# Kernel optimization log

Measured on AMD Instinct MI355X. Metric: run time of the kernel, lower is better.

## Reference

```python
import jax, jax.numpy as jnp
import numpy as np

INFO = 32  # info_dim


def _resort_perm(new_shape, cluster, old_num_cols):
    # Replicates resort(): column c of resort_mat has its single 1 at row perm[c],
    # so x @ resort_mat == x[..., perm]. (Faithfully reproduces the original
    # old_idx arithmetic, including its old_num_cols choice.)
    n0, n1 = new_shape
    perm = np.zeros(n0 * n1, np.int32)
    counter = 0
    for i in range(n0):
        for j in range(n1):
            filter_idx = (i % cluster[0]) * cluster[0] + (j % cluster[1])
            cluster_idx = (i // cluster[0]) * (n1 // cluster[1]) + (j // cluster[1])
            perm[counter] = filter_idx * old_num_cols + cluster_idx
            counter += 1
    return perm


def setup_inputs() -> dict:
    key = jax.random.key(0)
    ks = iter(jax.random.split(key, 64))
    def w(shape, scale=0.1):
        return jax.random.normal(next(ks), shape, dtype=jnp.float32) * scale
    B = 512
    inp = {"channel": jax.random.normal(next(ks), (B, 10, 16), dtype=jnp.float32)}
    for name, cin in [("l1", 10), ("g1", 10), ("l2", 2 * INFO), ("g2", 2 * INFO),
                      ("l4", 2 * INFO), ("g4", 2 * INFO), ("l5", 2 * INFO), ("g5", 2 * INFO),
                      ("l7", 2 * INFO), ("g7", 2 * INFO)]:
        inp["w_" + name] = w((INFO, cin))
        inp["b_" + name] = w((INFO,))
    for name in ["l3", "g3", "l6", "g6"]:
        inp["w_" + name] = w((9, INFO, 2 * INFO))
        inp["b_" + name] = w((9, INFO))
    inp["w_l8"] = w((1, 2 * INFO))
    inp["b_l8"] = w((1,))
    inp["perm3"] = jnp.asarray(_resort_perm((12, 12), (3, 3), 12))
    inp["perm6"] = jnp.asarray(_resort_perm((36, 36), (3, 3), 108))
    return inp


def _conv1(x, w, b):  # 1x1 Conv1d: [B,C,N] x [O,C] -> [B,O,N]
    return jnp.einsum('bcn,oc->bon', x, w) + b[None, :, None]


def _mean_bcast(x):
    # x @ (ones(N,N)/N) == broadcast mean over width (global_info_... = True)
    return jnp.broadcast_to(x.mean(axis=-1, keepdims=True), x.shape)


def _process_layer(x, wl, bl, wg, bg):
    fl = jax.nn.relu(_conv1(x, wl, bl))
    fg = _mean_bcast(jax.nn.relu(_conv1(x, wg, bg)))
    return jnp.concatenate([fl, fg], axis=1)


def _process_interp(x, wl, bl, wg, bg, perm):
    # wl/wg: [9,O,C]; per-filter [B,2*INFO,N] outputs concatenated along width,
    # then resorted (the one-hot permutation matmul becomes a gather).
    fl = jax.nn.relu(jnp.einsum('bcn,foc->fbon', x, wl) + bl[:, None, :, None])
    fg = _mean_bcast(jax.nn.relu(jnp.einsum('bcn,foc->fbon', x, wg) + bg[:, None, :, None]))
    cat = jnp.concatenate([fl, fg], axis=2)  # [9,B,2*INFO,N]
    f, b, c, n = cat.shape
    wide = jnp.transpose(cat, (1, 2, 0, 3)).reshape(b, c, f * n)  # [B,2*INFO,9N]
    return wide[:, :, perm]


def reference(channel, w_l1, b_l1, w_g1, b_g1, w_l2, b_l2, w_g2, b_g2,
              w_l3, b_l3, w_g3, b_g3, w_l4, b_l4, w_g4, b_g4,
              w_l5, b_l5, w_g5, b_g5, w_l6, b_l6, w_g6, b_g6,
              w_l7, b_l7, w_g7, b_g7, w_l8, b_l8, perm3, perm6):
    f = _process_layer(channel, w_l1, b_l1, w_g1, b_g1)        # [B,64,16]
    f = _process_layer(f, w_l2, b_l2, w_g2, b_g2)              # [B,64,16]
    f = _process_interp(f, w_l3, b_l3, w_g3, b_g3, perm3)      # [B,64,144]
    f = _process_layer(f, w_l4, b_l4, w_g4, b_g4)              # [B,64,144]
    f = _process_layer(f, w_l5, b_l5, w_g5, b_g5)              # [B,64,144]
    f = _process_interp(f, w_l6, b_l6, w_g6, b_g6, perm6)      # [B,64,1296]
    f = _process_layer(f, w_l7, b_l7, w_g7, b_g7)              # [B,64,1296]
    return _conv1(f, w_l8, b_l8) * np.pi                       # [B,1,1296]
```

## Files before the change

### kernel.cpp

```cpp
#include <hip/hip_runtime.h>
#include <math.h>

#define PI_F 3.14159265358979323846f
#define XQS 580
#define XB_B 4640

__device__ __forceinline__ void conv32K(
    const float* __restrict__ Wh,
    const float* __restrict__ xin,
    float* __restrict__ xout,
    const float* __restrict__ m0, const float* __restrict__ m1, const float* __restrict__ m2,
    const float* __restrict__ m3, const float* __restrict__ m4, const float* __restrict__ m5,
    float* __restrict__ xmsOut, int lane, int wid_u)
{
    int isg = wid_u >= 4, rb = (wid_u & 3) * 8;
    int rowbase = isg * 32 + rb;
    int cA = lane, cB = 64 + lane, cC = 128 + (lane & 15);
    float a0[8], a1[8], a2[8], a3[8], a4[8], a5[8];
    #pragma unroll
    for (int i = 0; i < 8; ++i) { a0[i]=0.f;a1[i]=0.f;a2[i]=0.f;a3[i]=0.f;a4[i]=0.f;a5[i]=0.f; }
    #pragma unroll 1
    for (int kb = 0; kb < 4; ++kb) {
        int ca = kb*2, cb = kb*2 + 1;
        float4 xA0 = *(const float4*)&xin[ca*XQS + cA*4];
        float4 xA1 = *(const float4*)&xin[cb*XQS + cA*4];
        float4 xB0 = *(const float4*)&xin[ca*XQS + cB*4];
        float4 xB1 = *(const float4*)&xin[cb*XQS + cB*4];
        float4 xC0 = *(const float4*)&xin[ca*XQS + cC*4];
        float4 xC1 = *(const float4*)&xin[cb*XQS + cC*4];
        float4 yA0 = *(const float4*)&xin[XB_B + ca*XQS + cA*4];
        float4 yA1 = *(const float4*)&xin[XB_B + cb*XQS + cA*4];
        float4 yB0 = *(const float4*)&xin[XB_B + ca*XQS + cB*4];
        float4 yB1 = *(const float4*)&xin[XB_B + cb*XQS + cB*4];
        float4 yC0 = *(const float4*)&xin[XB_B + ca*XQS + cC*4];
        float4 yC1 = *(const float4*)&xin[XB_B + cb*XQS + cC*4];
        const float* wb = Wh + rowbase*32 + kb*8;
        #pragma unroll
        for (int oi = 0; oi < 8; ++oi) {
            float4 w0 = *(const float4*)&wb[oi*32];
            float4 w1 = *(const float4*)&wb[oi*32 + 4];
            a0[oi] = fmaf(w0.x,xA0.x,a0[oi]); a0[oi] = fmaf(w0.y,xA0.y,a0[oi]);
            a0[oi] = fmaf(w0.z,xA0.z,a0[oi]); a0[oi] = fmaf(w0.w,xA0.w,a0[oi]);
            a0[oi] = fmaf(w1.x,xA1.x,a0[oi]); a0[oi] = fmaf(w1.y,xA1.y,a0[oi]);
            a0[oi] = fmaf(w1.z,xA1.z,a0[oi]); a0[oi] = fmaf(w1.w,xA1.w,a0[oi]);
            a1[oi] = fmaf(w0.x,xB0.x,a1[oi]); a1[oi] = fmaf(w0.y,xB0.y,a1[oi]);
            a1[oi] = fmaf(w0.z,xB0.z,a1[oi]); a1[oi] = fmaf(w0.w,xB0.w,a1[oi]);
            a1[oi] = fmaf(w1.x,xB1.x,a1[oi]); a1[oi] = fmaf(w1.y,xB1.y,a1[oi]);
            a1[oi] = fmaf(w1.z,xB1.z,a1[oi]); a1[oi] = fmaf(w1.w,xB1.w,a1[oi]);
            a2[oi] = fmaf(w0.x,xC0.x,a2[oi]); a2[oi] = fmaf(w0.y,xC0.y,a2[oi]);
            a2[oi] = fmaf(w0.z,xC0.z,a2[oi]); a2[oi] = fmaf(w0.w,xC0.w,a2[oi]);
            a2[oi] = fmaf(w1.x,xC1.x,a2[oi]); a2[oi] = fmaf(w1.y,xC1.y,a2[oi]);
            a2[oi] = fmaf(w1.z,xC1.z,a2[oi]); a2[oi] = fmaf(w1.w,xC1.w,a2[oi]);
            a3[oi] = fmaf(w0.x,yA0.x,a3[oi]); a3[oi] = fmaf(w0.y,yA0.y,a3[oi]);
            a3[oi] = fmaf(w0.z,yA0.z,a3[oi]); a3[oi] = fmaf(w0.w,yA0.w,a3[oi]);
            a3[oi] = fmaf(w1.x,yA1.x,a3[oi]); a3[oi] = fmaf(w1.y,yA1.y,a3[oi]);
            a3[oi] = fmaf(w1.z,yA1.z,a3[oi]); a3[oi] = fmaf(w1.w,yA1.w,a3[oi]);
            a4[oi] = fmaf(w0.x,yB0.x,a4[oi]); a4[oi] = fmaf(w0.y,yB0.y,a4[oi]);
            a4[oi] = fmaf(w0.z,yB0.z,a4[oi]); a4[oi] = fmaf(w0.w,yB0.w,a4[oi]);
            a4[oi] = fmaf(w1.x,yB1.x,a4[oi]); a4[oi] = fmaf(w1.y,yB1.y,a4[oi]);
            a4[oi] = fmaf(w1.z,yB1.z,a4[oi]); a4[oi] = fmaf(w1.w,yB1.w,a4[oi]);
            a5[oi] = fmaf(w0.x,yC0.x,a5[oi]); a5[oi] = fmaf(w0.y,yC0.y,a5[oi]);
            a5[oi] = fmaf(w0.z,yC0.z,a5[oi]); a5[oi] = fmaf(w0.w,yC0.w,a5[oi]);
            a5[oi] = fmaf(w1.x,yC1.x,a5[oi]); a5[oi] = fmaf(w1.y,yC1.y,a5[oi]);
            a5[oi] = fmaf(w1.z,yC1.z,a5[oi]); a5[oi] = fmaf(w1.w,yC1.w,a5[oi]);
        }
    }
    #pragma unroll
    for (int oi = 0; oi < 8; ++oi) {
        int row = rowbase + oi;
        a0[oi] = fmaxf(a0[oi] + m0[row], 0.f);
        a1[oi] = fmaxf(a1[oi] + m1[row], 0.f);
        a2[oi] = fmaxf(a2[oi] + m2[row], 0.f);
        a3[oi] = fmaxf(a3[oi] + m3[row], 0.f);
        a4[oi] = fmaxf(a4[oi] + m4[row], 0.f);
        a5[oi] = fmaxf(a5[oi] + m5[row], 0.f);
    }
    if (!isg) {
        int q0 = rb >> 2;
        *(float4*)&xout[ q0   *XQS + cA*4] = make_float4(a0[0],a0[1],a0[2],a0[3]);
        *(float4*)&xout[(q0+1)*XQS + cA*4] = make_float4(a0[4],a0[5],a0[6],a0[7]);
        *(float4*)&xout[ q0   *XQS + cB*4] = make_float4(a1[0],a1[1],a1[2],a1[3]);
        *(float4*)&xout[(q0+1)*XQS + cB*4] = make_float4(a1[4],a1[5],a1[6],a1[7]);
        *(float4*)&xout[XB_B +  q0   *XQS + cA*4] = make_float4(a3[0],a3[1],a3[2],a3[3]);
        *(float4*)&xout[XB_B + (q0+1)*XQS + cA*4] = make_float4(a3[4],a3[5],a3[6],a3[7]);
        *(float4*)&xout[XB_B +  q0   *XQS + cB*4] = make_float4(a4[0],a4[1],a4[2],a4[3]);
        *(float4*)&xout[XB_B + (q0+1)*XQS + cB*4] = make_float4(a4[4],a4[5],a4[6],a4[7]);
        if (lane < 16) {
            *(float4*)&xout[ q0   *XQS + cC*4] = make_float4(a2[0],a2[1],a2[2],a2[3]);
            *(float4*)&xout[(q0+1)*XQS + cC*4] = make_float4(a2[4],a2[5],a2[6],a2[7]);
            *(float4*)&xout[XB_B +  q0   *XQS + cC*4] = make_float4(a5[0],a5[1],a5[2],a5[3]);
            *(float4*)&xout[XB_B + (q0+1)*XQS + cC*4] = make_float4(a5[4],a5[5],a5[6],a5[7]);
        }
    } else {
        #pragma unroll
        for (int oi = 0; oi < 8; ++oi) {
            float s0 = a0[oi] + a1[oi] + ((lane < 16) ? a2[oi] : 0.f);
            float s1 = a3[oi] + a4[oi] + ((lane < 16) ? a5[oi] : 0.f);
            #pragma unroll
            for (int off = 1; off < 64; off <<= 1) { s0 += __shfl_xor(s0, off); s1 += __shfl_xor(s1, off); }
            if (lane == 0) { xmsOut[rb + oi] = s0 * (1.f/144.f); xmsOut[32 + rb + oi] = s1 * (1.f/144.f); }
        }
    }
}

__global__ __launch_bounds__(512, 2) void kfull(
    const float* __restrict__ ch,
    const float* __restrict__ wl1, const float* __restrict__ bl1,
    const float* __restrict__ wg1, const float* __restrict__ bg1,
    const float* __restrict__ wl2, const float* __restrict__ bl2,
    const float* __restrict__ wg2, const float* __restrict__ bg2,
    const float* __restrict__ wl3, const float* __restrict__ bl3,
    const float* __restrict__ wg3, const float* __restrict__ bg3,
    const float* __restrict__ wl4, const float* __restrict__ bl4,
    const float* __restrict__ wg4, const float* __restrict__ bg4,
    const float* __restrict__ wl5, const float* __restrict__ bl5,
    const float* __restrict__ wg5, const float* __restrict__ bg5,
    const float* __restrict__ wl6, const float* __restrict__ bl6,
    const float* __restrict__ wg6, const float* __restrict__ bg6,
    const float* __restrict__ wl7, const float* __restrict__ bl7,
    const float* __restrict__ wg7, const float* __restrict__ bg7,
    const float* __restrict__ wl8, const float* __restrict__ bl8,
    const int* __restrict__ perm3, const int* __restrict__ perm6,
    float* __restrict__ out)
{
    __shared__ float U[14336];
    __shared__ float xB[9280];
    __shared__ float W45h[4096];
    __shared__ float W7s[2048];
    __shared__ float mp4[896];
    __shared__ float mp5[128];
    __shared__ float mp6[448];
    __shared__ float mpg6[448];
    __shared__ float sgf[896];
    __shared__ float g6m[448];
    __shared__ float wl8s[64];
    __shared__ float xms4[64];
    __shared__ float xms5[64];
    __shared__ float l8v[2016];
    __shared__ int   pml[1296];
    __shared__ int   cnt[1008];
    __shared__ int   pfn3[144];
    __shared__ float redbuf[16];
    __shared__ float CbS[2];

    const int tid = threadIdx.x, lane = tid & 63, wid = tid >> 6;
    const int blk = blockIdx.x;
    const int wid_u = __builtin_amdgcn_readfirstlane(wid);

    float* f1s   = U;
    float* gts   = U + 2048;
    float* f2l   = U + 3072;
    float* cat3T = U + 5120;
    float* g3m   = U + 12352;
    float* xls   = U + 12814;
    float* x4s   = U;
    float* wg6h  = U;
    float* wl6h  = U + 7168;

    for (int t = tid; t < 1024; t += 512) {
        int l = t >> 9, rem = t & 511;
        int row = rem >> 3, q = rem & 7;
        const float* src = l ? ((row < 32) ? wl5 + row*64 : wg5 + (row-32)*64)
                             : ((row < 32) ? wl4 + row*64 : wg4 + (row-32)*64);
        *(float4*)&W45h[l*2048 + row*32 + q*4] = *(const float4*)&src[q*4];
    }
    {
        int row = tid >> 3, q = tid & 7;
        const float* src = (row < 32) ? (wl7 + row*64) : (wg7 + (row-32)*64);
        *(float4*)&W7s[row*32 + q*4] = *(const float4*)&src[q*4];
    }
    if (tid < 64) wl8s[tid] = wl8[tid];
    if (tid < 320) { int b = tid >= 160, i = tid - b*160; xls[b*160 + i] = ch[(2*blk + b)*160 + i]; }
    if (tid < 144) pfn3[tid] = perm3[tid];
    for (int t = tid; t < 1008; t += 512) cnt[t] = 0;
    __syncthreads();

    for (int t = tid; t < 1296; t += 512) { int p = perm6[t]; pml[t] = p; atomicAdd(&cnt[p], 1); }
    #pragma unroll
    for (int it = 0; it < 4; ++it) {
        int t = tid + it*512; int b = t >> 10, o = (t >> 4) & 63, n = t & 15;
        int isg = o >= 32, oo = o & 31;
        const float* w = isg ? wg1 : wl1;
        float acc = (isg ? bg1 : bl1)[oo];
        #pragma unroll
        for (int c = 0; c < 10; ++c) acc = fmaf(w[oo*10+c], xls[b*160 + c*16+n], acc);
        acc = fmaxf(acc, 0.f);
        if (isg) gts[b*512 + oo*16+n] = acc; else f1s[b*1024 + o*16+n] = acc;
    }
    __syncthreads();
    if (tid < 64) {
        int b = tid >> 5, j = tid & 31;
        float s = 0.f;
        #pragma unroll
        for (int n = 0; n < 16; ++n) s += gts[b*512 + j*16+n];
        s *= (1.f/16.f);
        #pragma unroll
        for (int n = 0; n < 16; ++n) f1s[b*1024 + (32+j)*16+n] = s;
    }
    __syncthreads();

    #pragma unroll
    for (int it = 0; it < 4; ++it) {
        int t = tid + it*512; int b = t >> 10, o = (t >> 4) & 63, n = t & 15;
        int isg = o >= 32, oo = o & 31;
        const float* w = isg ? wg2 : wl2;
        float acc = (isg ? bg2 : bl2)[oo];
        #pragma unroll
        for (int c = 0; c < 64; ++c) acc = fmaf(w[oo*64+c], f1s[b*1024 + c*16+n], acc);
        acc = fmaxf(acc, 0.f);
        if (isg) gts[b*512 + oo*16+n] = acc; else f2l[b*1024 + o*16+n] = acc;
    }
    __syncthreads();
    if (tid < 64) {
        int b = tid >> 5, j = tid & 31;
        float s = 0.f;
        #pragma unroll
        for (int n = 0; n < 16; ++n) s += gts[b*512 + j*16+n];
        s *= (1.f/16.f);
        #pragma unroll
        for (int n = 0; n < 16; ++n) f2l[b*1024 + (32+j)*16+n] = s;
    }
    __syncthreads();

    {
        int n16 = lane & 15, cs = lane >> 4;
        float xr0[16], xr1[16];
        #pragma unroll
        for (int i = 0; i < 16; ++i) {
            xr0[i] = f2l[cs*256 + i*16 + n16];
            xr1[i] = f2l[1024 + cs*256 + i*16 + n16];
        }
        int isg = wid_u >= 4;
        #pragma unroll 2
        for (int k = 0; k < 56; ++k) {
            int r = wid_u*56 + k;
            int rr = isg ? r - 224 : r;
            const float* wrow = (isg ? wg3 : wl3) + rr*64 + cs*16;
            float p0 = 0.f, p1 = 0.f;
            #pragma unroll
            for (int q = 0; q < 4; ++q) {
                float4 w = ((const float4*)wrow)[q];
                p0 = fmaf(w.x, xr0[q*4+0], p0); p0 = fmaf(w.y, xr0[q*4+1], p0);
                p0 = fmaf(w.z, xr0[q*4+2], p0); p0 = fmaf(w.w, xr0[q*4+3], p0);
                p1 = fmaf(w.x, xr1[q*4+0], p1); p1 = fmaf(w.y, xr1[q*4+1], p1);
                p1 = fmaf(w.z, xr1[q*4+2], p1); p1 = fmaf(w.w, xr1[q*4+3], p1);
            }
            p0 += __shfl_xor(p0, 16); p0 += __shfl_xor(p0, 32);
            p1 += __shfl_xor(p1, 16); p1 += __shfl_xor(p1, 32);
            float bb = (isg ? bg3 : bl3)[rr];
            p0 = fmaxf(p0 + bb, 0.f); p1 = fmaxf(p1 + bb, 0.f);
            if (!isg) {
                if (cs == 0) { cat3T[n16*226 + rr] = p0; cat3T[3616 + n16*226 + rr] = p1; }
            } else {
                p0 += __shfl_xor(p0, 1); p0 += __shfl_xor(p0, 2);
                p0 += __shfl_xor(p0, 4); p0 += __shfl_xor(p0, 8);
                p1 += __shfl_xor(p1, 1); p1 += __shfl_xor(p1, 2);
                p1 += __shfl_xor(p1, 4); p1 += __shfl_xor(p1, 8);
                if (lane == 0) {
                    g3m[(rr >> 5)*33 + (rr & 31)] = p0 * (1.f/16.f);
                    g3m[231 + (rr >> 5)*33 + (rr & 31)] = p1 * (1.f/16.f);
                }
            }
        }
    }
    __syncthreads();

    for (int t = tid; t < 9216; t += 512) {
        int b = t / 4608, rem = t - b*4608;
        int c4 = rem / 576, r2 = rem - c4*576;
        int col = r2 >> 2, ci = r2 & 3, c = c4*4 + ci;
        int p3 = pfn3[col]; int pf = p3 >> 4, pn = p3 & 15;
        xB[b*XB_B + c4*XQS + col*4 + ci] = cat3T[b*3616 + pn*226 + pf*32 + c];
    }
    for (int t = tid; t < 896; t += 512) {
        int b = t >= 448, t2 = t - b*448;
        int pf = t2 >> 6, row = t2 & 63;
        const float* w = ((row < 32) ? wl4 + row*64 : wg4 + (row-32)*64) + 32;
        float s = (row < 32) ? bl4[row] : bg4[row-32];
        #pragma unroll
        for (int q = 0; q < 8; ++q) {
            float4 wv = ((const float4*)w)[q];
            s = fmaf(wv.x, g3m[b*231 + pf*33 + q*4+0], s);
            s = fmaf(wv.y, g3m[b*231 + pf*33 + q*4+1], s);
            s = fmaf(wv.z, g3m[b*231 + pf*33 + q*4+2], s);
            s = fmaf(wv.w, g3m[b*231 + pf*33 + q*4+3], s);
        }
        mp4[b*448 + pf*64 + row] = s;
    }
    __syncthreads();

    {
        int pA = pfn3[lane] >> 4;
        int pB = pfn3[64 + lane] >> 4;
        int pC = pfn3[128 + (lane & 15)] >> 4;
        conv32K(W45h, xB, x4s,
                mp4 + pA*64, mp4 + pB*64, mp4 + pC*64,
                mp4 + 448 + pA*64, mp4 + 448 + pB*64, mp4 + 448 + pC*64,
                xms4, lane, wid_u);
    }
    __syncthreads();
    if (tid < 128) {
        int b = tid >= 64, row = tid & 63;
        const float* w = ((row < 32) ? wl5 + row*64 : wg5 + (row-32)*64) + 32;
        float s = (row < 32) ? bl5[row] : bg5[row-32];
        #pragma unroll
        for (int q = 0; q < 8; ++q) {
            float4 wv = ((const float4*)w)[q];
            s = fmaf(wv.x, xms4[b*32 + q*4+0], s);
            s = fmaf(wv.y, xms4[b*32 + q*4+1], s);
            s = fmaf(wv.z, xms4[b*32 + q*4+2], s);
            s = fmaf(wv.w, xms4[b*32 + q*4+3], s);
        }
        mp5[tid] = s;
    }
    __syncthreads();
    conv32K(W45h + 2048, x4s, xB,
            mp5, mp5, mp5, mp5 + 64, mp5 + 64, mp5 + 64,
            xms5, lane, wid_u);
    __syncthreads();

    #pragma unroll
    for (int k = 0; k < 7; ++k) {
        int t = tid + k*512;
        int half = t >= 1792, t2 = t - half*1792;
        int row = t2 >> 3, q = t2 & 7;
        const float* src = half ? (wl6 + row*64) : (wg6 + row*64);
        *(float4*)&U[half*7168 + row*32 + q*4] = *(const float4*)&src[q*4];
    }
    for (int t = tid; t < 896; t += 512) {
        int b = t >= 448, t2 = t - b*448;
        int isw = t2 >= 224, row = t2 - isw*224;
        const float* w = (isw ? wl6 + row*64 : wg6 + row*64) + 32;
        float s = isw ? bl6[row] : bg6[row];
        #pragma unroll
        for (int q = 0; q < 8; ++q) {
            float4 wv = ((const float4*)w)[q];
            s = fmaf(wv.x, xms5[b*32 + q*4+0], s);
            s = fmaf(wv.y, xms5[b*32 + q*4+1], s);
            s = fmaf(wv.z, xms5[b*32 + q*4+2], s);
            s = fmaf(wv.w, xms5[b*32 + q*4+3], s);
        }
        if (isw) mp6[b*224 + row] = s; else mpg6[b*224 + row] = s;
    }
    __syncthreads();

    {
        int bb = wid_u >= 4, w4 = wid_u & 3;
        int r0 = w4 * 56;
        int c0 = lane, c1 = 64 + lane, c2 = 128 + (lane & 15);
        const float* xb = xB + bb*XB_B;
        float4 xc0[8], xc1[8], xc2[8];
        #pragma unroll
        for (int q = 0; q < 8; ++q) {
            xc0[q] = *(const float4*)&xb[q*XQS + c0*4];
            xc1[q] = *(const float4*)&xb[q*XQS + c1*4];
            xc2[q] = *(const float4*)&xb[q*XQS + c2*4];
        }
        #pragma unroll 1
        for (int k = 0; k < 56; ++k) {
            int r = r0 + k;
            const float* wr = wg6h + r*32;
            float bb0 = mpg6[bb*224 + r];
            float v0 = bb0, v1 = bb0, v2 = bb0;
            #pragma unroll
            for (int q = 0; q < 8; ++q) {
                float4 w = *(const float4*)&wr[q*4];
                v0 = fmaf(w.x,xc0[q].x,v0); v0 = fmaf(w.y,xc0[q].y,v0); v0 = fmaf(w.z,xc0[q].z,v0); v0 = fmaf(w.w,xc0[q].w,v0);
                v1 = fmaf(w.x,xc1[q].x,v1); v1 = fmaf(w.y,xc1[q].y,v1); v1 = fmaf(w.z,xc1[q].z,v1); v1 = fmaf(w.w,xc1[q].w,v1);
                v2 = fmaf(w.x,xc2[q].x,v2); v2 = fmaf(w.y,xc2[q].y,v2); v2 = fmaf(w.z,xc2[q].z,v2); v2 = fmaf(w.w,xc2[q].w,v2);
            }
            float s = fmaxf(v0,0.f) + fmaxf(v1,0.f) + ((lane < 16) ? fmaxf(v2,0.f) : 0.f);
            #pragma unroll
            for (int off = 1; off < 64; off <<= 1) s += __shfl_xor(s, off);
            if (lane == 0) g6m[bb*224 + r] = s * (1.f/144.f);
        }
    }
    __syncthreads();

    for (int t = tid; t < 896; t += 512) {
        int b = t >= 448, t2 = t - b*448;
        int f = t2 >> 6, o7 = t2 & 63;
        const float* w = ((o7 < 32) ? wl7 + o7*64 : wg7 + (o7-32)*64) + 32;
        float s = (o7 < 32) ? bl7[o7] : bg7[o7-32];
        #pragma unroll
        for (int q = 0; q < 8; ++q) {
            float4 wv = ((const float4*)w)[q];
            s = fmaf(wv.x, g6m[b*224 + f*32 + q*4+0], s);
            s = fmaf(wv.y, g6m[b*224 + f*32 + q*4+1], s);
            s = fmaf(wv.z, g6m[b*224 + f*32 + q*4+2], s);
            s = fmaf(wv.w, g6m[b*224 + f*32 + q*4+3], s);
        }
        sgf[b*448 + f*64 + o7] = s;
    }
    __syncthreads();

    float gacc0 = 0.f, gacc1 = 0.f;
    {
        int t = 8*wid_u + (lane >> 3);
        bool valid = t < 63;
        int tt = valid ? t : 62;
        int f = tt / 9, g = tt - f*9;
        int colA = g*16 + (lane & 7), colB = colA + 8;
        const float* wfh = wl6h + f*1024;

        float a0A[32], a0B[32], a1A[32], a1B[32];
        #pragma unroll
        for (int o = 0; o < 32; ++o) { a0A[o]=0.f; a0B[o]=0.f; a1A[o]=0.f; a1B[o]=0.f; }
        #pragma unroll 1
        for (int kb = 0; kb < 4; ++kb) {
            int ca = kb*2, cb = kb*2 + 1;
            float4 xA0 = *(const float4*)&xB[ca*XQS + colA*4];
            float4 xA1 = *(const float4*)&xB[cb*XQS + colA*4];
            float4 xB0 = *(const float4*)&xB[ca*XQS + colB*4];
            float4 xB1 = *(const float4*)&xB[cb*XQS + colB*4];
            float4 yA0 = *(const float4*)&xB[XB_B + ca*XQS + colA*4];
            float4 yA1 = *(const float4*)&xB[XB_B + cb*XQS + colA*4];
            float4 yB0 = *(const float4*)&xB[XB_B + ca*XQS + colB*4];
            float4 yB1 = *(const float4*)&xB[XB_B + cb*XQS + colB*4];
            const float* wb = wfh + kb*8;
            #pragma unroll
            for (int o = 0; o < 32; ++o) {
                float4 w0 = *(const float4*)&wb[o*32];
                float4 w1 = *(const float4*)&wb[o*32 + 4];
                a0A[o] = fmaf(w0.x,xA0.x,a0A[o]); a0A[o] = fmaf(w0.y,xA0.y,a0A[o]);
                a0A[o] = fmaf(w0.z,xA0.z,a0A[o]); a0A[o] = fmaf(w0.w,xA0.w,a0A[o]);
                a0A[o] = fmaf(w1.x,xA1.x,a0A[o]); a0A[o] = fmaf(w1.y,xA1.y,a0A[o]);
                a0A[o] = fmaf(w1.z,xA1.z,a0A[o]); a0A[o] = fmaf(w1.w,xA1.w,a0A[o]);
                a0B[o] = fmaf(w0.x,xB0.x,a0B[o]); a0B[o] = fmaf(w0.y,xB0.y,a0B[o]);
                a0B[o] = fmaf(w0.z,xB0.z,a0B[o]); a0B[o] = fmaf(w0.w,xB0.w,a0B[o]);
                a0B[o] = fmaf(w1.x,xB1.x,a0B[o]); a0B[o] = fmaf(w1.y,xB1.y,a0B[o]);
                a0B[o] = fmaf(w1.z,xB1.z,a0B[o]); a0B[o] = fmaf(w1.w,xB1.w,a0B[o]);
                a1A[o] = fmaf(w0.x,yA0.x,a1A[o]); a1A[o] = fmaf(w0.y,yA0.y,a1A[o]);
                a1A[o] = fmaf(w0.z,yA0.z,a1A[o]); a1A[o] = fmaf(w0.w,yA0.w,a1A[o]);
                a1A[o] = fmaf(w1.x,yA1.x,a1A[o]); a1A[o] = fmaf(w1.y,yA1.y,a1A[o]);
                a1A[o] = fmaf(w1.z,yA1.z,a1A[o]); a1A[o] = fmaf(w1.w,yA1.w,a1A[o]);
                a1B[o] = fmaf(w0.x,yB0.x,a1B[o]); a1B[o] = fmaf(w0.y,yB0.y,a1B[o]);
                a1B[o] = fmaf(w0.z,yB0.z,a1B[o]); a1B[o] = fmaf(w0.w,yB0.w,a1B[o]);
                a1B[o] = fmaf(w1.x,yB1.x,a1B[o]); a1B[o] = fmaf(w1.y,yB1.y,a1B[o]);
                a1B[o] = fmaf(w1.z,yB1.z,a1B[o]); a1B[o] = fmaf(w1.w,yB1.w,a1B[o]);
            }
        }
        #pragma unroll
        for (int o = 0; o < 32; ++o) {
            float m0 = mp6[f*32 + o], m1 = mp6[224 + f*32 + o];
            a0A[o] = fmaxf(a0A[o] + m0, 0.f);
            a0B[o] = fmaxf(a0B[o] + m0, 0.f);
            a1A[o] = fmaxf(a1A[o] + m1, 0.f);
            a1B[o] = fmaxf(a1B[o] + m1, 0.f);
        }
        const float* sg0 = sgf + f*64;
        const float* sg1 = sgf + 448 + f*64;
        float l80A = 0.f, l80B = 0.f, l81A = 0.f, l81B = 0.f;
        float g0A = 0.f, g0B = 0.f, g1A = 0.f, g1B = 0.f;
        #pragma unroll 1
        for (int o7 = 0; o7 < 32; ++o7) {
            float s0 = sg0[o7], s1 = sg1[o7];
            float sA0 = s0, sB0 = s0, sA1 = s1, sB1 = s1;
            const float* wr = W7s + o7*32;
            #pragma unroll
            for (int q = 0; q < 8; ++q) {
                float4 w = *(const float4*)&wr[q*4];
                sA0 = fmaf(w.x,a0A[q*4+0],sA0); sA0 = fmaf(w.y,a0A[q*4+1],sA0);
                sA0 = fmaf(w.z,a0A[q*4+2],sA0); sA0 = fmaf(w.w,a0A[q*4+3],sA0);
                sB0 = fmaf(w.x,a0B[q*4+0],sB0); sB0 = fmaf(w.y,a0B[q*4+1],sB0);
                sB0 = fmaf(w.z,a0B[q*4+2],sB0); sB0 = fmaf(w.w,a0B[q*4+3],sB0);
                sA1 = fmaf(w.x,a1A[q*4+0],sA1); sA1 = fmaf(w.y,a1A[q*4+1],sA1);
                sA1 = fmaf(w.z,a1A[q*4+2],sA1); sA1 = fmaf(w.w,a1A[q*4+3],sA1);
                sB1 = fmaf(w.x,a1B[q*4+0],sB1); sB1 = fmaf(w.y,a1B[q*4+1],sB1);
                sB1 = fmaf(w.z,a1B[q*4+2],sB1); sB1 = fmaf(w.w,a1B[q*4+3],sB1);
            }
            float wgt = wl8s[o7];
            l80A = fmaf(wgt, fmaxf(sA0,0.f), l80A);
            l80B = fmaf(wgt, fmaxf(sB0,0.f), l80B);
            l81A = fmaf(wgt, fmaxf(sA1,0.f), l81A);
            l81B = fmaf(wgt, fmaxf(sB1,0.f), l81B);
        }
        #pragma unroll 1
        for (int o7 = 0; o7 < 32; ++o7) {
            float s0 = sg0[32+o7], s1 = sg1[32+o7];
            float sA0 = s0, sB0 = s0, sA1 = s1, sB1 = s1;
            const float* wr = W7s + (32+o7)*32;
            #pragma unroll
            for (int q = 0; q < 8; ++q) {
                float4 w = *(const float4*)&wr[q*4];
                sA0 = fmaf(w.x,a0A[q*4+0],sA0); sA0 = fmaf(w.y,a0A[q*4+1],sA0);
                sA0 = fmaf(w.z,a0A[q*4+2],sA0); sA0 = fmaf(w.w,a0A[q*4+3],sA0);
                sB0 = fmaf(w.x,a0B[q*4+0],sB0); sB0 = fmaf(w.y,a0B[q*4+1],sB0);
                sB0 = fmaf(w.z,a0B[q*4+2],sB0); sB0 = fmaf(w.w,a0B[q*4+3],sB0);
                sA1 = fmaf(w.x,a1A[q*4+0],sA1); sA1 = fmaf(w.y,a1A[q*4+1],sA1);
                sA1 = fmaf(w.z,a1A[q*4+2],sA1); sA1 = fmaf(w.w,a1A[q*4+3],sA1);
                sB1 = fmaf(w.x,a1B[q*4+0],sB1); sB1 = fmaf(w.y,a1B[q*4+1],sB1);
                sB1 = fmaf(w.z,a1B[q*4+2],sB1); sB1 = fmaf(w.w,a1B[q*4+3],sB1);
            }
            float wgt = wl8s[32+o7];
            g0A = fmaf(wgt, fmaxf(sA0,0.f), g0A);
            g0B = fmaf(wgt, fmaxf(sB0,0.f), g0B);
            g1A = fmaf(wgt, fmaxf(sA1,0.f), g1A);
            g1B = fmaf(wgt, fmaxf(sB1,0.f), g1B);
        }
        if (valid) {
            l8v[f*144 + colA] = l80A;
            l8v[f*144 + colB] = l80B;
            l8v[1008 + f*144 + colA] = l81A;
            l8v[1008 + f*144 + colB] = l81B;
            gacc0 = fmaf((float)cnt[f*144 + colA], g0A, gacc0);
            gacc0 = fmaf((float)cnt[f*144 + colB], g0B, gacc0);
            gacc1 = fmaf((float)cnt[f*144 + colA], g1A, gacc1);
            gacc1 = fmaf((float)cnt[f*144 + colB], g1B, gacc1);
        }
    }

    #pragma unroll
    for (int off = 32; off > 0; off >>= 1) { gacc0 += __shfl_down(gacc0, off); gacc1 += __shfl_down(gacc1, off); }
    if (lane == 0) { redbuf[wid] = gacc0; redbuf[8 + wid] = gacc1; }
    __syncthreads();
    if (tid < 2) {
        float s = 0.f;
        #pragma unroll
        for (int i = 0; i < 8; ++i) s += redbuf[tid*8 + i];
        CbS[tid] = bl8[0] + s * (1.f/1296.f);
    }
    __syncthreads();
    for (int t = tid; t < 2592; t += 512) {
        int b = t >= 1296, idx = t - b*1296;
        out[(2*blk + b)*1296 + idx] = PI_F * (l8v[b*1008 + pml[idx]] + CbS[b]);
    }
}

extern "C" void kernel_launch(void* const* d_in, const int* in_sizes, int n_in,
                              void* d_out, int out_size, void* d_ws, size_t ws_size,
                              hipStream_t stream) {
    (void)in_sizes; (void)n_in; (void)out_size; (void)d_ws; (void)ws_size;
    const float* ch  = (const float*)d_in[0];
    const float* wl1 = (const float*)d_in[1];  const float* bl1v = (const float*)d_in[2];
    const float* wg1 = (const float*)d_in[3];  const float* bg1v = (const float*)d_in[4];
    const float* wl2 = (const float*)d_in[5];  const float* bl2v = (const float*)d_in[6];
    const float* wg2 = (const float*)d_in[7];  const float* bg2v = (const float*)d_in[8];
    const float* wl4 = (const float*)d_in[9];  const float* bl4v = (const float*)d_in[10];
    const float* wg4 = (const float*)d_in[11]; const float* bg4v = (const float*)d_in[12];
    const float* wl5 = (const float*)d_in[13]; const float* bl5v = (const float*)d_in[14];
    const float* wg5 = (const float*)d_in[15]; const float* bg5v = (const float*)d_in[16];
    const float* wl7 = (const float*)d_in[17]; const float* bl7v = (const float*)d_in[18];
    const float* wg7 = (const float*)d_in[19]; const float* bg7v = (const float*)d_in[20];
    const float* wl3 = (const float*)d_in[21]; const float* bl3v = (const float*)d_in[22];
    const float* wg3 = (const float*)d_in[23]; const float* bg3v = (const float*)d_in[24];
    const float* wl6 = (const float*)d_in[25]; const float* bl6v = (const float*)d_in[26];
    const float* wg6 = (const float*)d_in[27]; const float* bg6v = (const float*)d_in[28];
    const float* wl8 = (const float*)d_in[29]; const float* bl8v = (const float*)d_in[30];
    const int* perm3 = (const int*)d_in[31];
    const int* perm6 = (const int*)d_in[32];
    float* out = (float*)d_out;

    kfull<<<256, 512, 0, stream>>>(ch,
        wl1, bl1v, wg1, bg1v, wl2, bl2v, wg2, bg2v,
        wl3, bl3v, wg3, bg3v, wl4, bl4v, wg4, bg4v,
        wl5, bl5v, wg5, bg5v, wl6, bl6v, wg6, bg6v,
        wl7, bl7v, wg7, bg7v, wl8, bl8v, perm3, perm6, out);
}
```

Baseline: 265.1 us.

## Double block size to 1024 threads and halve per-wave work in all stages

The fused kernel now launches 1024 threads per block instead of 512 and redistributes every stage so each wave handles half as many output rows (4 instead of 8 in conv32K, 28 instead of 56 in the interp stages). The aim is more waves in flight per CU to hide LDS and global latency, plus fewer registers per thread. Some stages (the final l8 section) are still limited to 512 threads, so half the block idles there. Only one block fits per CU because of the large shared memory, so the gain depends on the extra waves within that block.

```diff
diff --git a/kernel.cpp b/kernel.cpp
--- a/kernel.cpp
+++ b/kernel.cpp
@@ -4,6 +4,7 @@
 #define PI_F 3.14159265358979323846f
 #define XQS 580
 #define XB_B 4640
+#define BS 1024
 
 __device__ __forceinline__ void conv32K(
     const float* __restrict__ Wh,
@@ -13,12 +14,13 @@
     const float* __restrict__ m3, const float* __restrict__ m4, const float* __restrict__ m5,
     float* __restrict__ xmsOut, int lane, int wid_u)
 {
-    int isg = wid_u >= 4, rb = (wid_u & 3) * 8;
+    int isg = wid_u >= 8, rb = (wid_u & 7) * 4;
     int rowbase = isg * 32 + rb;
+    int q0 = rowbase >> 2;
     int cA = lane, cB = 64 + lane, cC = 128 + (lane & 15);
-    float a0[8], a1[8], a2[8], a3[8], a4[8], a5[8];
+    float a0[4], a1[4], a2[4], a3[4], a4[4], a5[4];
     #pragma unroll
-    for (int i = 0; i < 8; ++i) { a0[i]=0.f;a1[i]=0.f;a2[i]=0.f;a3[i]=0.f;a4[i]=0.f;a5[i]=0.f; }
+    for (int i = 0; i < 4; ++i) { a0[i]=0.f;a1[i]=0.f;a2[i]=0.f;a3[i]=0.f;a4[i]=0.f;a5[i]=0.f; }
     #pragma unroll 1
     for (int kb = 0; kb < 4; ++kb) {
         int ca = kb*2, cb = kb*2 + 1;
@@ -36,7 +38,7 @@
         float4 yC1 = *(const float4*)&xin[XB_B + cb*XQS + cC*4];
         const float* wb = Wh + rowbase*32 + kb*8;
         #pragma unroll
-        for (int oi = 0; oi < 8; ++oi) {
+        for (int oi = 0; oi < 4; ++oi) {
             float4 w0 = *(const float4*)&wb[oi*32];
             float4 w1 = *(const float4*)&wb[oi*32 + 4];
             a0[oi] = fmaf(w0.x,xA0.x,a0[oi]); a0[oi] = fmaf(w0.y,xA0.y,a0[oi]);
@@ -66,7 +68,7 @@
         }
     }
     #pragma unroll
-    for (int oi = 0; oi < 8; ++oi) {
+    for (int oi = 0; oi < 4; ++oi) {
         int row = rowbase + oi;
         a0[oi] = fmaxf(a0[oi] + m0[row], 0.f);
         a1[oi] = fmaxf(a1[oi] + m1[row], 0.f);
@@ -76,24 +78,17 @@
         a5[oi] = fmaxf(a5[oi] + m5[row], 0.f);
     }
     if (!isg) {
-        int q0 = rb >> 2;
-        *(float4*)&xout[ q0   *XQS + cA*4] = make_float4(a0[0],a0[1],a0[2],a0[3]);
-        *(float4*)&xout[(q0+1)*XQS + cA*4] = make_float4(a0[4],a0[5],a0[6],a0[7]);
-        *(float4*)&xout[ q0   *XQS + cB*4] = make_float4(a1[0],a1[1],a1[2],a1[3]);
-        *(float4*)&xout[(q0+1)*XQS + cB*4] = make_float4(a1[4],a1[5],a1[6],a1[7]);
-        *(float4*)&xout[XB_B +  q0   *XQS + cA*4] = make_float4(a3[0],a3[1],a3[2],a3[3]);
-        *(float4*)&xout[XB_B + (q0+1)*XQS + cA*4] = make_float4(a3[4],a3[5],a3[6],a3[7]);
-        *(float4*)&xout[XB_B +  q0   *XQS + cB*4] = make_float4(a4[0],a4[1],a4[2],a4[3]);
-        *(float4*)&xout[XB_B + (q0+1)*XQS + cB*4] = make_float4(a4[4],a4[5],a4[6],a4[7]);
+        *(float4*)&xout[q0*XQS + cA*4] = make_float4(a0[0],a0[1],a0[2],a0[3]);
+        *(float4*)&xout[q0*XQS + cB*4] = make_float4(a1[0],a1[1],a1[2],a1[3]);
+        *(float4*)&xout[XB_B + q0*XQS + cA*4] = make_float4(a3[0],a3[1],a3[2],a3[3]);
+        *(float4*)&xout[XB_B + q0*XQS + cB*4] = make_float4(a4[0],a4[1],a4[2],a4[3]);
         if (lane < 16) {
-            *(float4*)&xout[ q0   *XQS + cC*4] = make_float4(a2[0],a2[1],a2[2],a2[3]);
-            *(float4*)&xout[(q0+1)*XQS + cC*4] = make_float4(a2[4],a2[5],a2[6],a2[7]);
-            *(float4*)&xout[XB_B +  q0   *XQS + cC*4] = make_float4(a5[0],a5[1],a5[2],a5[3]);
-            *(float4*)&xout[XB_B + (q0+1)*XQS + cC*4] = make_float4(a5[4],a5[5],a5[6],a5[7]);
+            *(float4*)&xout[q0*XQS + cC*4] = make_float4(a2[0],a2[1],a2[2],a2[3]);
+            *(float4*)&xout[XB_B + q0*XQS + cC*4] = make_float4(a5[0],a5[1],a5[2],a5[3]);
         }
     } else {
         #pragma unroll
-        for (int oi = 0; oi < 8; ++oi) {
+        for (int oi = 0; oi < 4; ++oi) {
             float s0 = a0[oi] + a1[oi] + ((lane < 16) ? a2[oi] : 0.f);
             float s1 = a3[oi] + a4[oi] + ((lane < 16) ? a5[oi] : 0.f);
             #pragma unroll
@@ -103,7 +98,7 @@
     }
 }
 
-__global__ __launch_bounds__(512, 2) void kfull(
+__global__ __launch_bounds__(1024, 4) void kfull(
     const float* __restrict__ ch,
     const float* __restrict__ wl1, const float* __restrict__ bl1,
     const float* __restrict__ wg1, const float* __restrict__ bg1,
@@ -140,7 +135,7 @@
     __shared__ int   pml[1296];
     __shared__ int   cnt[1008];
     __shared__ int   pfn3[144];
-    __shared__ float redbuf[16];
+    __shared__ float redbuf[32];
     __shared__ float CbS[2];
 
     const int tid = threadIdx.x, lane = tid & 63, wid = tid >> 6;
@@ -157,14 +152,14 @@
     float* wg6h  = U;
     float* wl6h  = U + 7168;
 
-    for (int t = tid; t < 1024; t += 512) {
-        int l = t >> 9, rem = t & 511;
+    {
+        int l = tid >> 9, rem = tid & 511;
         int row = rem >> 3, q = rem & 7;
         const float* src = l ? ((row < 32) ? wl5 + row*64 : wg5 + (row-32)*64)
                              : ((row < 32) ? wl4 + row*64 : wg4 + (row-32)*64);
         *(float4*)&W45h[l*2048 + row*32 + q*4] = *(const float4*)&src[q*4];
     }
-    {
+    if (tid < 512) {
         int row = tid >> 3, q = tid & 7;
         const float* src = (row < 32) ? (wl7 + row*64) : (wg7 + (row-32)*64);
         *(float4*)&W7s[row*32 + q*4] = *(const float4*)&src[q*4];
@@ -172,13 +167,13 @@
     if (tid < 64) wl8s[tid] = wl8[tid];
     if (tid < 320) { int b = tid >= 160, i = tid - b*160; xls[b*160 + i] = ch[(2*blk + b)*160 + i]; }
     if (tid < 144) pfn3[tid] = perm3[tid];
-    for (int t = tid; t < 1008; t += 512) cnt[t] = 0;
-    __syncthreads();
-
-    for (int t = tid; t < 1296; t += 512) { int p = perm6[t]; pml[t] = p; atomicAdd(&cnt[p], 1); }
+    if (tid < 1008) cnt[tid] = 0;
+    __syncthreads();
+
+    for (int t = tid; t < 1296; t += BS) { int p = perm6[t]; pml[t] = p; atomicAdd(&cnt[p], 1); }
     #pragma unroll
-    for (int it = 0; it < 4; ++it) {
-        int t = tid + it*512; int b = t >> 10, o = (t >> 4) & 63, n = t & 15;
+    for (int it = 0; it < 2; ++it) {
+        int t = tid + it*BS; int b = t >> 10, o = (t >> 4) & 63, n = t & 15;
         int isg = o >= 32, oo = o & 31;
         const float* w = isg ? wg1 : wl1;
         float acc = (isg ? bg1 : bl1)[oo];
@@ -200,8 +195,8 @@
     __syncthreads();
 
     #pragma unroll
-    for (int it = 0; it < 4; ++it) {
-        int t = tid + it*512; int b = t >> 10, o = (t >> 4) & 63, n = t & 15;
+    for (int it = 0; it < 2; ++it) {
+        int t = tid + it*BS; int b = t >> 10, o = (t >> 4) & 63, n = t & 15;
         int isg = o >= 32, oo = o & 31;
         const float* w = isg ? wg2 : wl2;
         float acc = (isg ? bg2 : bl2)[oo];
@@ -230,10 +225,10 @@
             xr0[i] = f2l[cs*256 + i*16 + n16];
             xr1[i] = f2l[1024 + cs*256 + i*16 + n16];
         }
-        int isg = wid_u >= 4;
+        int isg = wid_u >= 8;
         #pragma unroll 2
-        for (int k = 0; k < 56; ++k) {
-            int r = wid_u*56 + k;
+        for (int k = 0; k < 28; ++k) {
+            int r = wid_u*28 + k;
             int rr = isg ? r - 224 : r;
             const float* wrow = (isg ? wg3 : wl3) + rr*64 + cs*16;
             float p0 = 0.f, p1 = 0.f;
@@ -265,15 +260,15 @@
     }
     __syncthreads();
 
-    for (int t = tid; t < 9216; t += 512) {
+    for (int t = tid; t < 9216; t += BS) {
         int b = t / 4608, rem = t - b*4608;
         int c4 = rem / 576, r2 = rem - c4*576;
         int col = r2 >> 2, ci = r2 & 3, c = c4*4 + ci;
         int p3 = pfn3[col]; int pf = p3 >> 4, pn = p3 & 15;
         xB[b*XB_B + c4*XQS + col*4 + ci] = cat3T[b*3616 + pn*226 + pf*32 + c];
     }
-    for (int t = tid; t < 896; t += 512) {
-        int b = t >= 448, t2 = t - b*448;
+    if (tid < 896) {
+        int b = tid >= 448, t2 = tid - b*448;
         int pf = t2 >> 6, row = t2 & 63;
         const float* w = ((row < 32) ? wl4 + row*64 : wg4 + (row-32)*64) + 32;
         float s = (row < 32) ? bl4[row] : bg4[row-32];
@@ -320,15 +315,17 @@
     __syncthreads();
 
     #pragma unroll
-    for (int k = 0; k < 7; ++k) {
-        int t = tid + k*512;
-        int half = t >= 1792, t2 = t - half*1792;
-        int row = t2 >> 3, q = t2 & 7;
-        const float* src = half ? (wl6 + row*64) : (wg6 + row*64);
-        *(float4*)&U[half*7168 + row*32 + q*4] = *(const float4*)&src[q*4];
-    }
-    for (int t = tid; t < 896; t += 512) {
-        int b = t >= 448, t2 = t - b*448;
+    for (int k = 0; k < 4; ++k) {
+        int t = tid + k*BS;
+        if (t < 3584) {
+            int half = t >= 1792, t2 = t - half*1792;
+            int row = t2 >> 3, q = t2 & 7;
+            const float* src = half ? (wl6 + row*64) : (wg6 + row*64);
+            *(float4*)&U[half*7168 + row*32 + q*4] = *(const float4*)&src[q*4];
+        }
+    }
+    if (tid < 896) {
+        int b = tid >= 448, t2 = tid - b*448;
         int isw = t2 >= 224, row = t2 - isw*224;
         const float* w = (isw ? wl6 + row*64 : wg6 + row*64) + 32;
         float s = isw ? bl6[row] : bg6[row];
@@ -345,8 +342,8 @@
     __syncthreads();
 
     {
-        int bb = wid_u >= 4, w4 = wid_u & 3;
-        int r0 = w4 * 56;
+        int bb = wid_u >= 8, w8 = wid_u & 7;
+        int r0 = w8 * 28;
         int c0 = lane, c1 = 64 + lane, c2 = 128 + (lane & 15);
         const float* xb = xB + bb*XB_B;
         float4 xc0[8], xc1[8], xc2[8];
@@ -357,7 +354,7 @@
             xc2[q] = *(const float4*)&xb[q*XQS + c2*4];
         }
         #pragma unroll 1
-        for (int k = 0; k < 56; ++k) {
+        for (int k = 0; k < 28; ++k) {
             int r = r0 + k;
             const float* wr = wg6h + r*32;
             float bb0 = mpg6[bb*224 + r];
@@ -377,8 +374,8 @@
     }
     __syncthreads();
 
-    for (int t = tid; t < 896; t += 512) {
-        int b = t >= 448, t2 = t - b*448;
+    if (tid < 896) {
+        int b = tid >= 448, t2 = tid - b*448;
         int f = t2 >> 6, o7 = t2 & 63;
         const float* w = ((o7 < 32) ? wl7 + o7*64 : wg7 + (o7-32)*64) + 32;
         float s = (o7 < 32) ? bl7[o7] : bg7[o7-32];
@@ -395,7 +392,7 @@
     __syncthreads();
 
     float gacc0 = 0.f, gacc1 = 0.f;
-    {
+    if (tid < 512) {
         int t = 8*wid_u + (lane >> 3);
         bool valid = t < 63;
         int tt = valid ? t : 62;
@@ -512,16 +509,16 @@
 
     #pragma unroll
     for (int off = 32; off > 0; off >>= 1) { gacc0 += __shfl_down(gacc0, off); gacc1 += __shfl_down(gacc1, off); }
-    if (lane == 0) { redbuf[wid] = gacc0; redbuf[8 + wid] = gacc1; }
+    if (lane == 0) { redbuf[wid] = gacc0; redbuf[16 + wid] = gacc1; }
     __syncthreads();
     if (tid < 2) {
         float s = 0.f;
         #pragma unroll
-        for (int i = 0; i < 8; ++i) s += redbuf[tid*8 + i];
+        for (int i = 0; i < 16; ++i) s += redbuf[tid*16 + i];
         CbS[tid] = bl8[0] + s * (1.f/1296.f);
     }
     __syncthreads();
-    for (int t = tid; t < 2592; t += 512) {
+    for (int t = tid; t < 2592; t += BS) {
         int b = t >= 1296, idx = t - b*1296;
         out[(2*blk + b)*1296 + idx] = PI_F * (l8v[b*1008 + pml[idx]] + CbS[b]);
     }
@@ -551,7 +548,7 @@
     const int* perm6 = (const int*)d_in[32];
     float* out = (float*)d_out;
 
-    kfull<<<256, 512, 0, stream>>>(ch,
+    kfull<<<256, 1024, 0, stream>>>(ch,
         wl1, bl1v, wg1, bg1v, wl2, bl2v, wg2, bg2v,
         wl3, bl3v, wg3, bg3v, wl4, bl4v, wg4, bg4v,
         wl5, bl5v, wg5, bg5v, wl6, bl6v, wg6, bg6v,
```

After: 374.7 us. 1.41x slower.
